# Optimization experiments

Hardware: AMD Instinct MI355X
Metric: run time of the kernel (lower is better)

The kernel has to match this reference:

```python
import jax, jax.numpy as jnp
import numpy as np

NEG_INF = -1e10

def setup_inputs() -> dict:
    key = jax.random.key(0)
    k1, k2, k3, k4, k5, k6 = jax.random.split(key, 6)
    B, S, DEC, ENC, A = 64, 4096, 512, 1024, 256
    return {
        "decoder_hidden": jax.random.normal(k1, (B, DEC), dtype=jnp.float32),
        "encoder_outputs": jax.random.normal(k2, (B, S, ENC), dtype=jnp.float32),
        "mask": jax.random.randint(k3, (B, S), 0, 2).astype(jnp.bool_),
        "W_dec": jax.random.normal(k4, (DEC, A), dtype=jnp.float32) * 0.05,
        "W_enc": jax.random.normal(k5, (ENC, A), dtype=jnp.float32) * 0.05,
        "v": jax.random.normal(k6, (A,), dtype=jnp.float32) * 0.05,
    }

def reference(decoder_hidden, encoder_outputs, mask, W_dec, W_enc, v):
    # decoder projection: (B, A) -> broadcast over src_len
    dec_proj = decoder_hidden @ W_dec                      # (B, A)
    enc_proj = jnp.einsum('bse,ea->bsa', encoder_outputs, W_enc)  # (B, S, A)
    # additive score: v . tanh(dec + enc)
    scores = jnp.einsum('bsa,a->bs', jnp.tanh(dec_proj[:, None, :] + enc_proj), v)  # (B, S)
    scores = jnp.where(mask, NEG_INF, scores)
    attention_weights = jax.nn.softmax(scores, axis=1)     # (B, S)
    context_vector = jnp.einsum('bs,bse->be', attention_weights, encoder_outputs)  # (B, ENC)
    return (context_vector, attention_weights)
```

## Files before the change

kernel.cpp:

```cpp
#include <hip/hip_runtime.h>
#include <hip/hip_bf16.h>
#include <math.h>

typedef __bf16 bf16_t;
typedef __bf16 bf16x8 __attribute__((ext_vector_type(8)));
typedef __bf16 bf16x4 __attribute__((ext_vector_type(4)));
typedef float f32x4 __attribute__((ext_vector_type(4)));


__global__ __launch_bounds__(256) void k_dec_proj(const float* __restrict__ dh,
                                                  const float* __restrict__ Wd,
                                                  float* __restrict__ dec_proj) {
    int b = blockIdx.x, a = threadIdx.x;
    const float* dhb = dh + b * 512;
    float acc = 0.f;
    #pragma unroll 8
    for (int k = 0; k < 512; ++k) acc += dhb[k] * Wd[k * 256 + a];
    dec_proj[b * 256 + a] = acc;
}

__global__ __launch_bounds__(256) void k_wenc_t(const float* __restrict__ Wenc,
                                                bf16_t* __restrict__ WencT) {
    __shared__ float tile[64][65];
    int k0 = blockIdx.x * 64, a0 = blockIdx.y * 64, tid = threadIdx.x;
    #pragma unroll
    for (int it = 0; it < 16; ++it) {
        int e = it * 256 + tid;
        int kk = e >> 6, aa = e & 63;
        tile[kk][aa] = Wenc[(k0 + kk) * 256 + a0 + aa];
    }
    __syncthreads();
    #pragma unroll
    for (int it = 0; it < 16; ++it) {
        int e = it * 256 + tid;
        int aa = e >> 6, kk = e & 63;
        WencT[(size_t)(a0 + aa) * 1024 + k0 + kk] = (bf16_t)tile[kk][aa];
    }
}

__global__ __launch_bounds__(256) void k_scores(const float* __restrict__ enc,
                                                const bf16_t* __restrict__ WencT,
                                                const float* __restrict__ dec_proj,
                                                const float* __restrict__ v,
                                                float* __restrict__ scores) {
    __shared__ bf16_t Abuf[64][72];
    __shared__ bf16_t Bbuf[256][72];
    __shared__ float dec_s[256];
    __shared__ float v_s[256];
    __shared__ float score_s[64];

    const int tid  = threadIdx.x;
    const int R    = blockIdx.x * 64;
    const int b    = R >> 12;
    const int wv   = tid >> 6;
    const int lane = tid & 63;
    const int lr   = lane & 15;
    const int lg   = lane >> 4;

    dec_s[tid] = dec_proj[b * 256 + tid];
    v_s[tid]   = v[tid];
    if (tid < 64) score_s[tid] = 0.f;

    f32x4 zero = {0.f, 0.f, 0.f, 0.f};
    f32x4 acc[4][4];
    #pragma unroll
    for (int i = 0; i < 4; ++i)
        #pragma unroll
        for (int j = 0; j < 4; ++j) acc[i][j] = zero;

    const float* encR = enc + (size_t)R * 1024;

    for (int kb = 0; kb < 16; ++kb) {
        __syncthreads();
        #pragma unroll
        for (int rep = 0; rep < 4; ++rep) {
            int idx = rep * 256 + tid;
            int row = idx >> 4, c4 = idx & 15;
            const float4 val = *(const float4*)(encR + (size_t)row * 1024 + kb * 64 + c4 * 4);
            bf16x4 o;
            o.x = (bf16_t)val.x; o.y = (bf16_t)val.y; o.z = (bf16_t)val.z; o.w = (bf16_t)val.w;
            *(bf16x4*)&Abuf[row][c4 * 4] = o;
        }
        #pragma unroll
        for (int rep = 0; rep < 8; ++rep) {
            int idx = rep * 256 + tid;
            int arow = idx >> 3, c8 = idx & 7;
            *(bf16x8*)&Bbuf[arow][c8 * 8] =
                *(const bf16x8*)(WencT + (size_t)arow * 1024 + kb * 64 + c8 * 8);
        }
        __syncthreads();
        #pragma unroll
        for (int kk = 0; kk < 2; ++kk) {
            const int ko = kk * 32 + lg * 8;
            bf16x8 af[4], bfr[4];
            #pragma unroll
            for (int tm = 0; tm < 4; ++tm) af[tm] = *(const bf16x8*)&Abuf[tm * 16 + lr][ko];
            #pragma unroll
            for (int tn = 0; tn < 4; ++tn) bfr[tn] = *(const bf16x8*)&Bbuf[wv * 64 + tn * 16 + lr][ko];
            #pragma unroll
            for (int tm = 0; tm < 4; ++tm)
                #pragma unroll
                for (int tn = 0; tn < 4; ++tn)
                    acc[tm][tn] = __builtin_amdgcn_mfma_f32_16x16x32_bf16(af[tm], bfr[tn], acc[tm][tn], 0, 0, 0);
        }
    }

    #pragma unroll
    for (int tm = 0; tm < 4; ++tm) {
        #pragma unroll
        for (int r = 0; r < 4; ++r) {
            float sum = 0.f;
            #pragma unroll
            for (int tn = 0; tn < 4; ++tn) {
                int col = wv * 64 + tn * 16 + lr;
                sum += v_s[col] * tanhf(dec_s[col] + acc[tm][tn][r]);
            }
            sum += __shfl_xor(sum, 1);
            sum += __shfl_xor(sum, 2);
            sum += __shfl_xor(sum, 4);
            sum += __shfl_xor(sum, 8);
            if (lr == 0) atomicAdd(&score_s[tm * 16 + lg * 4 + r], sum);
        }
    }
    __syncthreads();
    if (tid < 64) scores[R + tid] = score_s[tid];
}

__global__ __launch_bounds__(256) void k_softmax(float* __restrict__ sw,
                                                 const int* __restrict__ mask) {
    int b = blockIdx.x, tid = threadIdx.x;
    float vals[16];
    float mx = -3.0e38f;
    #pragma unroll
    for (int i = 0; i < 16; ++i) {
        int s = i * 256 + tid;
        float sc = sw[b * 4096 + s];
        if (mask[b * 4096 + s] != 0) sc = -1e10f;
        vals[i] = sc;
        mx = fmaxf(mx, sc);
    }
    #pragma unroll
    for (int off = 1; off < 64; off <<= 1) mx = fmaxf(mx, __shfl_xor(mx, off));
    __shared__ float red[4];
    __shared__ float red2[4];
    if ((tid & 63) == 0) red[tid >> 6] = mx;
    __syncthreads();
    mx = fmaxf(fmaxf(red[0], red[1]), fmaxf(red[2], red[3]));
    float sum = 0.f;
    #pragma unroll
    for (int i = 0; i < 16; ++i) { vals[i] = __expf(vals[i] - mx); sum += vals[i]; }
    #pragma unroll
    for (int off = 1; off < 64; off <<= 1) sum += __shfl_xor(sum, off);
    if ((tid & 63) == 0) red2[tid >> 6] = sum;
    __syncthreads();
    sum = red2[0] + red2[1] + red2[2] + red2[3];
    float inv = 1.0f / sum;
    #pragma unroll
    for (int i = 0; i < 16; ++i) sw[b * 4096 + i * 256 + tid] = vals[i] * inv;
}

__global__ __launch_bounds__(256) void k_ctx(const float* __restrict__ enc,
                                             const float* __restrict__ w,
                                             float* __restrict__ partial) {
    int chunk = blockIdx.x, b = blockIdx.y, tid = threadIdx.x;
    float4 acc = {0.f, 0.f, 0.f, 0.f};
    int s0 = chunk * 256;
    const float* base = enc + ((size_t)b * 4096 + s0) * 1024 + tid * 4;
    const float* wb = w + b * 4096 + s0;
    #pragma unroll 4
    for (int i = 0; i < 256; ++i) {
        float ww = wb[i];
        float4 e = *(const float4*)(base + (size_t)i * 1024);
        acc.x += ww * e.x; acc.y += ww * e.y; acc.z += ww * e.z; acc.w += ww * e.w;
    }
    *(float4*)(partial + ((size_t)chunk * 64 + b) * 1024 + tid * 4) = acc;
}

__global__ __launch_bounds__(256) void k_comb(const float* __restrict__ partial,
                                              float* __restrict__ outc) {
    int idx = blockIdx.x * 256 + threadIdx.x;
    float s = 0.f;
    #pragma unroll
    for (int c = 0; c < 16; ++c) s += partial[c * 65536 + idx];
    outc[idx] = s;
}

extern "C" void kernel_launch(void* const* d_in, const int* in_sizes, int n_in,
                              void* d_out, int out_size, void* d_ws, size_t ws_size,
                              hipStream_t stream) {
    const float* dh   = (const float*)d_in[0];
    const float* enc  = (const float*)d_in[1];
    const int*   mask = (const int*)d_in[2];
    const float* Wd   = (const float*)d_in[3];
    const float* Wenc = (const float*)d_in[4];
    const float* v    = (const float*)d_in[5];

    float* out  = (float*)d_out;
    float* outc = out;
    float* outw = out + 65536;

    float* ws_f     = (float*)d_ws;
    float* dec_proj = ws_f;
    float* partial  = ws_f + 16384;
    bf16_t* WencT   = (bf16_t*)(ws_f + 16384 + 1048576);

    k_dec_proj<<<64, 256, 0, stream>>>(dh, Wd, dec_proj);
    k_wenc_t<<<dim3(16, 4), 256, 0, stream>>>(Wenc, WencT);
    k_scores<<<4096, 256, 0, stream>>>(enc, WencT, dec_proj, v, outw);
    k_softmax<<<64, 256, 0, stream>>>(outw, mask);
    k_ctx<<<dim3(16, 64), 256, 0, stream>>>(enc, outw, partial);
    k_comb<<<256, 256, 0, stream>>>(partial, outc);
}
```

Before: 1.650 ms.

## Fuse score, softmax numerator and context accumulation into one pass over encoder

The score kernel now computes exp(score) without max subtraction, writes per-block partial sums, and accumulates the weighted context from the 64-row encoder tile it just loaded. Separate kernels then normalise the context and the weights. This cuts the second full read of the 1 GB encoder tensor by the context kernel and also replaces tanhf with an exp-based tanh. In exchange the softmax is not max-stabilised, so large scores could overflow, and masked rows are skipped by testing for zero weights.

```diff
diff --git a/kernel.cpp b/kernel.cpp
--- a/kernel.cpp
+++ b/kernel.cpp
@@ -7,6 +7,10 @@
 typedef __bf16 bf16x4 __attribute__((ext_vector_type(4)));
 typedef float f32x4 __attribute__((ext_vector_type(4)));
 
+
+__device__ __forceinline__ float fast_tanh(float x) {
+    return 1.0f - 2.0f / (__expf(2.0f * x) + 1.0f);
+}
 
 __global__ __launch_bounds__(256) void k_dec_proj(const float* __restrict__ dh,
                                                   const float* __restrict__ Wd,
@@ -38,11 +42,15 @@
     }
 }
 
-__global__ __launch_bounds__(256) void k_scores(const float* __restrict__ enc,
-                                                const bf16_t* __restrict__ WencT,
-                                                const float* __restrict__ dec_proj,
-                                                const float* __restrict__ v,
-                                                float* __restrict__ scores) {
+__global__ __launch_bounds__(256) void k_fused(const float* __restrict__ enc,
+                                               const bf16_t* __restrict__ WencT,
+                                               const float* __restrict__ dec_proj,
+                                               const float* __restrict__ v,
+                                               const int* __restrict__ mask,
+                                               float* __restrict__ ew,
+                                               float* __restrict__ esum,
+                                               float* __restrict__ partial)
+{
     __shared__ bf16_t Abuf[64][72];
     __shared__ bf16_t Bbuf[256][72];
     __shared__ float dec_s[256];
@@ -113,7 +121,7 @@
             #pragma unroll
             for (int tn = 0; tn < 4; ++tn) {
                 int col = wv * 64 + tn * 16 + lr;
-                sum += v_s[col] * tanhf(dec_s[col] + acc[tm][tn][r]);
+                sum += v_s[col] * fast_tanh(dec_s[col] + acc[tm][tn][r]);
             }
             sum += __shfl_xor(sum, 1);
             sum += __shfl_xor(sum, 2);
@@ -123,66 +131,57 @@
         }
     }
     __syncthreads();
-    if (tid < 64) scores[R + tid] = score_s[tid];
-}
-
-__global__ __launch_bounds__(256) void k_softmax(float* __restrict__ sw,
-                                                 const int* __restrict__ mask) {
-    int b = blockIdx.x, tid = threadIdx.x;
-    float vals[16];
-    float mx = -3.0e38f;
-    #pragma unroll
-    for (int i = 0; i < 16; ++i) {
-        int s = i * 256 + tid;
-        float sc = sw[b * 4096 + s];
-        if (mask[b * 4096 + s] != 0) sc = -1e10f;
-        vals[i] = sc;
-        mx = fmaxf(mx, sc);
-    }
-    #pragma unroll
-    for (int off = 1; off < 64; off <<= 1) mx = fmaxf(mx, __shfl_xor(mx, off));
-    __shared__ float red[4];
-    __shared__ float red2[4];
-    if ((tid & 63) == 0) red[tid >> 6] = mx;
+
+    if (tid < 64) {
+        float sc = score_s[tid];
+        if (mask[R + tid] != 0) sc = -1e10f;
+        float e = __expf(sc);
+        score_s[tid] = e;
+        ew[R + tid] = e;
+    }
     __syncthreads();
-    mx = fmaxf(fmaxf(red[0], red[1]), fmaxf(red[2], red[3]));
-    float sum = 0.f;
-    #pragma unroll
-    for (int i = 0; i < 16; ++i) { vals[i] = __expf(vals[i] - mx); sum += vals[i]; }
-    #pragma unroll
-    for (int off = 1; off < 64; off <<= 1) sum += __shfl_xor(sum, off);
-    if ((tid & 63) == 0) red2[tid >> 6] = sum;
-    __syncthreads();
-    sum = red2[0] + red2[1] + red2[2] + red2[3];
-    float inv = 1.0f / sum;
-    #pragma unroll
-    for (int i = 0; i < 16; ++i) sw[b * 4096 + i * 256 + tid] = vals[i] * inv;
-}
-
-__global__ __launch_bounds__(256) void k_ctx(const float* __restrict__ enc,
-                                             const float* __restrict__ w,
-                                             float* __restrict__ partial) {
-    int chunk = blockIdx.x, b = blockIdx.y, tid = threadIdx.x;
-    float4 acc = {0.f, 0.f, 0.f, 0.f};
-    int s0 = chunk * 256;
-    const float* base = enc + ((size_t)b * 4096 + s0) * 1024 + tid * 4;
-    const float* wb = w + b * 4096 + s0;
-    #pragma unroll 4
-    for (int i = 0; i < 256; ++i) {
-        float ww = wb[i];
-        float4 e = *(const float4*)(base + (size_t)i * 1024);
-        acc.x += ww * e.x; acc.y += ww * e.y; acc.z += ww * e.z; acc.w += ww * e.w;
-    }
-    *(float4*)(partial + ((size_t)chunk * 64 + b) * 1024 + tid * 4) = acc;
-}
-
-__global__ __launch_bounds__(256) void k_comb(const float* __restrict__ partial,
-                                              float* __restrict__ outc) {
-    int idx = blockIdx.x * 256 + threadIdx.x;
+
+    if (tid < 64) {
+        float e = score_s[tid];
+        #pragma unroll
+        for (int off = 1; off < 64; off <<= 1) e += __shfl_xor(e, off);
+        if (tid == 0) esum[blockIdx.x] = e;
+    }
+
+    f32x4 cacc = {0.f, 0.f, 0.f, 0.f};
+    const float* basep = encR + tid * 4;
+    for (int s = 0; s < 64; ++s) {
+        float e = score_s[s];
+        if (e != 0.f) {
+            float4 ev = *(const float4*)(basep + (size_t)s * 1024);
+            cacc.x += e * ev.x; cacc.y += e * ev.y; cacc.z += e * ev.z; cacc.w += e * ev.w;
+        }
+    }
+    *(f32x4*)(partial + (size_t)blockIdx.x * 1024 + tid * 4) = cacc;
+}
+
+__global__ __launch_bounds__(256) void k_ctx_comb(const float* __restrict__ partial,
+                                                  const float* __restrict__ esum,
+                                                  float* __restrict__ outc) {
+    int b = blockIdx.y, ec = blockIdx.x, tid = threadIdx.x;
+    int e = ec * 256 + tid;
+    float d = 0.f;
+    #pragma unroll
+    for (int c = 0; c < 64; ++c) d += esum[b * 64 + c];
     float s = 0.f;
-    #pragma unroll
-    for (int c = 0; c < 16; ++c) s += partial[c * 65536 + idx];
-    outc[idx] = s;
+    #pragma unroll 8
+    for (int c = 0; c < 64; ++c) s += partial[(size_t)(b * 64 + c) * 1024 + e];
+    outc[b * 1024 + e] = s / d;
+}
+
+__global__ __launch_bounds__(256) void k_wnorm(float* __restrict__ ew,
+                                               const float* __restrict__ esum) {
+    int b = blockIdx.y, sc = blockIdx.x, tid = threadIdx.x;
+    float d = 0.f;
+    #pragma unroll
+    for (int c = 0; c < 64; ++c) d += esum[b * 64 + c];
+    int s = sc * 256 + tid;
+    ew[b * 4096 + s] = ew[b * 4096 + s] / d;
 }
 
 extern "C" void kernel_launch(void* const* d_in, const int* in_sizes, int n_in,
@@ -199,15 +198,15 @@
     float* outc = out;
     float* outw = out + 65536;
 
-    float* ws_f     = (float*)d_ws;
-    float* dec_proj = ws_f;
-    float* partial  = ws_f + 16384;
-    bf16_t* WencT   = (bf16_t*)(ws_f + 16384 + 1048576);
+    char* ws = (char*)d_ws;
+    float*  dec_proj = (float*)(ws);
+    float*  esum     = (float*)(ws + 65536);
+    float*  partial  = (float*)(ws + 81920);
+    bf16_t* WencT    = (bf16_t*)(ws + 81920 + 16777216);
 
     k_dec_proj<<<64, 256, 0, stream>>>(dh, Wd, dec_proj);
     k_wenc_t<<<dim3(16, 4), 256, 0, stream>>>(Wenc, WencT);
-    k_scores<<<4096, 256, 0, stream>>>(enc, WencT, dec_proj, v, outw);
-    k_softmax<<<64, 256, 0, stream>>>(outw, mask);
-    k_ctx<<<dim3(16, 64), 256, 0, stream>>>(enc, outw, partial);
-    k_comb<<<256, 256, 0, stream>>>(partial, outc);
-}
+    k_fused<<<4096, 256, 0, stream>>>(enc, WencT, dec_proj, v, mask, outw, esum, partial);
+    k_ctx_comb<<<dim3(4, 64), 256, 0, stream>>>(partial, esum, outc);
+    k_wnorm<<<dim3(16, 64), 256, 0, stream>>>(outw, esum);
+}
```

Result: faster. 1.583 ms (-4.1%).
